# Kernel tuning notes

Hardware: AMD Instinct MI355X
Metric: run time of the kernel (lower is better)

## Reference

```python
import jax, jax.numpy as jnp
import numpy as np

N_LAYERS = 2
K_NEIGHBOURS = 30  # graph_top_K keeps k_neighbours + 1 entries per row
EPS = 1e-12        # torch F.normalize eps


def setup_inputs() -> dict:
    key = jax.random.key(0)
    k1, k2 = jax.random.split(key)
    N, d = 8192, 512
    x = jax.random.normal(k1, (N, d), dtype=jnp.float32)
    W = jax.random.normal(k2, (N_LAYERS, d, d), dtype=jnp.float32) * 0.02
    b = jnp.zeros((N_LAYERS, d), dtype=jnp.float32)
    return {"x": x, "W": W, "b": b}


def reference(x, W, b):
    # MLP: interval_forward -- relu between layers, linear on last layer
    h = x
    for i in range(N_LAYERS - 1):
        h = jax.nn.relu(h @ W[i].T + b[i])
    h = h @ W[N_LAYERS - 1].T + b[N_LAYERS - 1]

    # F.normalize(h, dim=-1, p=2)
    norm = jnp.linalg.norm(h, axis=-1, keepdims=True)
    h = h / jnp.maximum(norm, EPS)

    # cal_similarity_graph: dense N x N cosine similarity
    sim = h @ h.T  # [N, N]

    # graph_top_K(sim, k+1): keep top-(k+1) values per row, zero elsewhere
    k = K_NEIGHBOURS + 1
    vals, idx = jax.lax.top_k(sim, k)  # [N, k]
    N = sim.shape[0]
    masked = jnp.zeros_like(sim).at[jnp.arange(N)[:, None], idx].set(vals)

    # apply_non_linearity(x, 'relu', slope, alpha) -> relu
    return jax.nn.relu(masked)
```

## Files before the change

kernel.cpp:

```cpp
#include <hip/hip_runtime.h>
#include <hip/hip_bf16.h>

typedef __attribute__((ext_vector_type(8))) short bf16x8;
typedef __attribute__((ext_vector_type(8))) unsigned short u16x8;
typedef __attribute__((ext_vector_type(4))) float f32x4;

__global__ __launch_bounds__(256)
void gemm_nt(const float* __restrict__ A, const float* __restrict__ B,
             const float* __restrict__ bias, float* __restrict__ C,
             int M, int N, int K, int do_relu)
{
    constexpr int KS = 16;
    constexpr int LDT = 132;
    __shared__ float As[KS * LDT];
    __shared__ float Bs[KS * LDT];

    const int t    = threadIdx.x;
    const int row0 = blockIdx.y * 128;
    const int col0 = blockIdx.x * 128;
    const int tm   = t & 15;
    const int tn   = t >> 4;
    const int lrow = t >> 2;
    const int lk   = (t & 3) << 2;

    const float* Ap0 = A + (size_t)(row0 + lrow)      * K + lk;
    const float* Ap1 = A + (size_t)(row0 + lrow + 64) * K + lk;
    const float* Bp0 = B + (size_t)(col0 + lrow)      * K + lk;
    const float* Bp1 = B + (size_t)(col0 + lrow + 64) * K + lk;

    float4 a0 = *(const float4*)(Ap0);
    float4 a1 = *(const float4*)(Ap1);
    float4 b0 = *(const float4*)(Bp0);
    float4 b1 = *(const float4*)(Bp1);

    float acc[8][8];
#pragma unroll
    for (int i = 0; i < 8; ++i)
#pragma unroll
        for (int j = 0; j < 8; ++j) acc[i][j] = 0.f;

    for (int k0 = 0; k0 < K; k0 += KS) {
        __syncthreads();
        As[(lk + 0) * LDT + lrow] = a0.x;
        As[(lk + 1) * LDT + lrow] = a0.y;
        As[(lk + 2) * LDT + lrow] = a0.z;
        As[(lk + 3) * LDT + lrow] = a0.w;
        As[(lk + 0) * LDT + lrow + 64] = a1.x;
        As[(lk + 1) * LDT + lrow + 64] = a1.y;
        As[(lk + 2) * LDT + lrow + 64] = a1.z;
        As[(lk + 3) * LDT + lrow + 64] = a1.w;
        Bs[(lk + 0) * LDT + lrow] = b0.x;
        Bs[(lk + 1) * LDT + lrow] = b0.y;
        Bs[(lk + 2) * LDT + lrow] = b0.z;
        Bs[(lk + 3) * LDT + lrow] = b0.w;
        Bs[(lk + 0) * LDT + lrow + 64] = b1.x;
        Bs[(lk + 1) * LDT + lrow + 64] = b1.y;
        Bs[(lk + 2) * LDT + lrow + 64] = b1.z;
        Bs[(lk + 3) * LDT + lrow + 64] = b1.w;
        __syncthreads();
        if (k0 + KS < K) {
            a0 = *(const float4*)(Ap0 + k0 + KS);
            a1 = *(const float4*)(Ap1 + k0 + KS);
            b0 = *(const float4*)(Bp0 + k0 + KS);
            b1 = *(const float4*)(Bp1 + k0 + KS);
        }
#pragma unroll
        for (int kk = 0; kk < KS; ++kk) {
            const float4 av0 = *(const float4*)&As[kk * LDT + 8 * tm];
            const float4 av1 = *(const float4*)&As[kk * LDT + 8 * tm + 4];
            const float4 bv0 = *(const float4*)&Bs[kk * LDT + 8 * tn];
            const float4 bv1 = *(const float4*)&Bs[kk * LDT + 8 * tn + 4];
            const float a[8] = {av0.x, av0.y, av0.z, av0.w, av1.x, av1.y, av1.z, av1.w};
            const float bb[8] = {bv0.x, bv0.y, bv0.z, bv0.w, bv1.x, bv1.y, bv1.z, bv1.w};
#pragma unroll
            for (int i = 0; i < 8; ++i)
#pragma unroll
                for (int j = 0; j < 8; ++j)
                    acc[i][j] += a[i] * bb[j];
        }
    }

#pragma unroll
    for (int i = 0; i < 8; ++i) {
        const int r = row0 + 8 * tm + i;
        float* Crow = C + (size_t)r * N + col0 + 8 * tn;
        float o[8];
#pragma unroll
        for (int j = 0; j < 8; ++j) o[j] = acc[i][j];
        if (bias) {
#pragma unroll
            for (int j = 0; j < 8; ++j) o[j] += bias[col0 + 8 * tn + j];
        }
        if (do_relu) {
#pragma unroll
            for (int j = 0; j < 8; ++j) o[j] = fmaxf(o[j], 0.f);
        }
        float4 o0 = {o[0], o[1], o[2], o[3]};
        float4 o1 = {o[4], o[5], o[6], o[7]};
        *(float4*)(Crow)     = o0;
        *(float4*)(Crow + 4) = o1;
    }
}

__global__ __launch_bounds__(128)
void rownorm_split(const float* __restrict__ in, unsigned short* __restrict__ Hhi,
                   unsigned short* __restrict__ Hmid, unsigned short* __restrict__ Hlo)
{
    __shared__ float s[2];
    const int r = blockIdx.x, t = threadIdx.x;
    const float4 v = ((const float4*)(in + (size_t)r * 512))[t];
    float ss = v.x * v.x + v.y * v.y + v.z * v.z + v.w * v.w;
#pragma unroll
    for (int off = 32; off; off >>= 1) ss += __shfl_down(ss, off);
    if ((t & 63) == 0) s[t >> 6] = ss;
    __syncthreads();
    const float den = fmaxf(sqrtf(s[0] + s[1]), 1e-12f);
    const float f[4] = {v.x / den, v.y / den, v.z / den, v.w / den};
    ushort4 uh, um, ul;
    unsigned short* ph = (unsigned short*)&uh;
    unsigned short* pm = (unsigned short*)&um;
    unsigned short* pl = (unsigned short*)&ul;
#pragma unroll
    for (int j = 0; j < 4; ++j) {
        const __hip_bfloat16 h = __float2bfloat16(f[j]);
        const float fh = __bfloat162float(h);
        const float r1 = f[j] - fh;
        const __hip_bfloat16 m = __float2bfloat16(r1);
        const float fm = __bfloat162float(m);
        const float r2 = r1 - fm;
        const __hip_bfloat16 l = __float2bfloat16(r2);
        ph[j] = *(const unsigned short*)&h;
        pm[j] = *(const unsigned short*)&m;
        pl[j] = *(const unsigned short*)&l;
    }
    const size_t o = (size_t)r * 512 + 4 * t;
    *(ushort4*)(Hhi  + o) = uh;
    *(ushort4*)(Hmid + o) = um;
    *(ushort4*)(Hlo  + o) = ul;
}

__global__ __launch_bounds__(256)
void gemm_sym_mfma(const unsigned short* __restrict__ Hhi,
                   const unsigned short* __restrict__ Hmid,
                   const unsigned short* __restrict__ Hlo,
                   float* __restrict__ C, int Nn)
{
    constexpr int K  = 512;
    constexpr int KC = 32;
    constexpr int LR = 40;
    __shared__ unsigned short lds[6 * 128 * LR];

    const int q = blockIdx.x;
    int ct = (int)((sqrtf(8.0f * (float)q + 1.0f) - 1.0f) * 0.5f);
    while ((ct + 1) * (ct + 2) / 2 <= q) ++ct;
    while (ct * (ct + 1) / 2 > q) --ct;
    const int rt = q - ct * (ct + 1) / 2;
    const int row0 = rt * 128;
    const int col0 = ct * 128;

    const int t    = threadIdx.x;
    const int lane = t & 63;
    const int wid  = t >> 6;
    const int wr   = (wid >> 1) * 64;
    const int wc   = (wid & 1) * 64;

    const int r  = t >> 1;
    const int kh = (t & 1) * 16;
    const unsigned short* srcs[6] = {
        Hhi  + (size_t)(row0 + r) * K, Hmid + (size_t)(row0 + r) * K, Hlo + (size_t)(row0 + r) * K,
        Hhi  + (size_t)(col0 + r) * K, Hmid + (size_t)(col0 + r) * K, Hlo + (size_t)(col0 + r) * K };

    u16x8 pf[12];
#pragma unroll
    for (int a = 0; a < 6; ++a) {
        pf[2 * a]     = *(const u16x8*)(srcs[a] + kh);
        pf[2 * a + 1] = *(const u16x8*)(srcs[a] + kh + 8);
    }

    f32x4 acc[4][4];
#pragma unroll
    for (int i = 0; i < 4; ++i)
#pragma unroll
        for (int j = 0; j < 4; ++j) acc[i][j] = (f32x4){0.f, 0.f, 0.f, 0.f};

    const int fro = (lane & 15) * LR + 8 * (lane >> 4);

    for (int k0 = 0; k0 < K; k0 += KC) {
        __syncthreads();
#pragma unroll
        for (int a = 0; a < 6; ++a) {
            *(u16x8*)&lds[a * 128 * LR + r * LR + kh]     = pf[2 * a];
            *(u16x8*)&lds[a * 128 * LR + r * LR + kh + 8] = pf[2 * a + 1];
        }
        __syncthreads();
        if (k0 + KC < K) {
#pragma unroll
            for (int a = 0; a < 6; ++a) {
                pf[2 * a]     = *(const u16x8*)(srcs[a] + k0 + KC + kh);
                pf[2 * a + 1] = *(const u16x8*)(srcs[a] + k0 + KC + kh + 8);
            }
        }
        bf16x8 af[3][4], bf[3][4];
#pragma unroll
        for (int p = 0; p < 3; ++p)
#pragma unroll
            for (int ti = 0; ti < 4; ++ti) {
                af[p][ti] = *(const bf16x8*)&lds[p * 128 * LR + (wr + ti * 16) * LR + fro];
                bf[p][ti] = *(const bf16x8*)&lds[(3 + p) * 128 * LR + (wc + ti * 16) * LR + fro];
            }
#pragma unroll
        for (int ti = 0; ti < 4; ++ti)
#pragma unroll
            for (int tj = 0; tj < 4; ++tj) {
                f32x4 c = acc[ti][tj];
                c = __builtin_amdgcn_mfma_f32_16x16x32_bf16(af[0][ti], bf[0][tj], c, 0, 0, 0);
                c = __builtin_amdgcn_mfma_f32_16x16x32_bf16(af[0][ti], bf[1][tj], c, 0, 0, 0);
                c = __builtin_amdgcn_mfma_f32_16x16x32_bf16(af[1][ti], bf[0][tj], c, 0, 0, 0);
                c = __builtin_amdgcn_mfma_f32_16x16x32_bf16(af[1][ti], bf[1][tj], c, 0, 0, 0);
                c = __builtin_amdgcn_mfma_f32_16x16x32_bf16(af[0][ti], bf[2][tj], c, 0, 0, 0);
                c = __builtin_amdgcn_mfma_f32_16x16x32_bf16(af[2][ti], bf[0][tj], c, 0, 0, 0);
                acc[ti][tj] = c;
            }
    }

    const int crow = (lane >> 4) * 4;
    const int ccol = lane & 15;
#pragma unroll
    for (int ti = 0; ti < 4; ++ti)
#pragma unroll
        for (int tj = 0; tj < 4; ++tj)
#pragma unroll
            for (int qq = 0; qq < 4; ++qq) {
                const int rr = row0 + wr + ti * 16 + crow + qq;
                const int cc = col0 + wc + tj * 16 + ccol;
                C[(size_t)rr * Nn + cc] = acc[ti][tj][qq];
            }
    if (ct != rt) {
#pragma unroll
        for (int ti = 0; ti < 4; ++ti)
#pragma unroll
            for (int tj = 0; tj < 4; ++tj)
#pragma unroll
                for (int qq = 0; qq < 4; ++qq) {
                    const int rr = row0 + wr + ti * 16 + crow + qq;
                    const int cc = col0 + wc + tj * 16 + ccol;
                    C[(size_t)cc * Nn + rr] = acc[ti][tj][qq];
                }
    }
}

__global__ __launch_bounds__(128)
void rownorm(const float* __restrict__ in, float* __restrict__ out)
{
    __shared__ float s[2];
    const int r = blockIdx.x, t = threadIdx.x;
    const float4 v = ((const float4*)(in + (size_t)r * 512))[t];
    float ss = v.x * v.x + v.y * v.y + v.z * v.z + v.w * v.w;
#pragma unroll
    for (int off = 32; off; off >>= 1) ss += __shfl_down(ss, off);
    if ((t & 63) == 0) s[t >> 6] = ss;
    __syncthreads();
    const float den = fmaxf(sqrtf(s[0] + s[1]), 1e-12f);
    float4 o;
    o.x = v.x / den; o.y = v.y / den; o.z = v.z / den; o.w = v.w / den;
    ((float4*)(out + (size_t)r * 512))[t] = o;
}

__global__ __launch_bounds__(256)
void gemm_syn(const float* __restrict__ H, float* __restrict__ C, int Nn, int K)
{
    constexpr int KS = 16;
    constexpr int LDT = 132;
    __shared__ float As[KS * LDT];
    __shared__ float Bs[KS * LDT];

    const int q = blockIdx.x;
    int ct = (int)((sqrtf(8.0f * (float)q + 1.0f) - 1.0f) * 0.5f);
    while ((ct + 1) * (ct + 2) / 2 <= q) ++ct;
    while (ct * (ct + 1) / 2 > q) --ct;
    const int rt = q - ct * (ct + 1) / 2;
    const int row0 = rt * 128;
    const int col0 = ct * 128;

    const int t    = threadIdx.x;
    const int tm   = t & 15;
    const int tn   = t >> 4;
    const int lrow = t >> 2;
    const int lk   = (t & 3) << 2;

    const float* Ap0 = H + (size_t)(row0 + lrow)      * K + lk;
    const float* Ap1 = H + (size_t)(row0 + lrow + 64) * K + lk;
    const float* Bp0 = H + (size_t)(col0 + lrow)      * K + lk;
    const float* Bp1 = H + (size_t)(col0 + lrow + 64) * K + lk;

    float4 a0 = *(const float4*)(Ap0);
    float4 a1 = *(const float4*)(Ap1);
    float4 b0 = *(const float4*)(Bp0);
    float4 b1 = *(const float4*)(Bp1);

    float acc[8][8];
#pragma unroll
    for (int i = 0; i < 8; ++i)
#pragma unroll
        for (int j = 0; j < 8; ++j) acc[i][j] = 0.f;

    for (int k0 = 0; k0 < K; k0 += KS) {
        __syncthreads();
        As[(lk + 0) * LDT + lrow] = a0.x;
        As[(lk + 1) * LDT + lrow] = a0.y;
        As[(lk + 2) * LDT + lrow] = a0.z;
        As[(lk + 3) * LDT + lrow] = a0.w;
        As[(lk + 0) * LDT + lrow + 64] = a1.x;
        As[(lk + 1) * LDT + lrow + 64] = a1.y;
        As[(lk + 2) * LDT + lrow + 64] = a1.z;
        As[(lk + 3) * LDT + lrow + 64] = a1.w;
        Bs[(lk + 0) * LDT + lrow] = b0.x;
        Bs[(lk + 1) * LDT + lrow] = b0.y;
        Bs[(lk + 2) * LDT + lrow] = b0.z;
        Bs[(lk + 3) * LDT + lrow] = b0.w;
        Bs[(lk + 0) * LDT + lrow + 64] = b1.x;
        Bs[(lk + 1) * LDT + lrow + 64] = b1.y;
        Bs[(lk + 2) * LDT + lrow + 64] = b1.z;
        Bs[(lk + 3) * LDT + lrow + 64] = b1.w;
        __syncthreads();
        if (k0 + KS < K) {
            a0 = *(const float4*)(Ap0 + k0 + KS);
            a1 = *(const float4*)(Ap1 + k0 + KS);
            b0 = *(const float4*)(Bp0 + k0 + KS);
            b1 = *(const float4*)(Bp1 + k0 + KS);
        }
#pragma unroll
        for (int kk = 0; kk < KS; ++kk) {
            const float4 av0 = *(const float4*)&As[kk * LDT + 4 * tm];
            const float4 av1 = *(const float4*)&As[kk * LDT + 4 * tm + 64];
            const float4 bv0 = *(const float4*)&Bs[kk * LDT + 4 * tn];
            const float4 bv1 = *(const float4*)&Bs[kk * LDT + 4 * tn + 64];
            const float a[8] = {av0.x, av0.y, av0.z, av0.w, av1.x, av1.y, av1.z, av1.w};
            const float bb[8] = {bv0.x, bv0.y, bv0.z, bv0.w, bv1.x, bv1.y, bv1.z, bv1.w};
#pragma unroll
            for (int i = 0; i < 8; ++i)
#pragma unroll
                for (int j = 0; j < 8; ++j)
                    acc[i][j] += a[i] * bb[j];
        }
    }

#pragma unroll
    for (int ih = 0; ih < 2; ++ih)
#pragma unroll
    for (int i2 = 0; i2 < 4; ++i2) {
        const int rr = row0 + ih * 64 + 4 * tm + i2;
        float* Crow = C + (size_t)rr * Nn + col0;
        const int ia = ih * 4 + i2;
        float4 o0 = {acc[ia][0], acc[ia][1], acc[ia][2], acc[ia][3]};
        float4 o1 = {acc[ia][4], acc[ia][5], acc[ia][6], acc[ia][7]};
        *(float4*)(Crow + 4 * tn)      = o0;
        *(float4*)(Crow + 64 + 4 * tn) = o1;
    }
    if (ct != rt) {
#pragma unroll
        for (int jh = 0; jh < 2; ++jh)
#pragma unroll
        for (int j2 = 0; j2 < 4; ++j2) {
            const int rr = col0 + jh * 64 + 4 * tn + j2;
            float* Crow = C + (size_t)rr * Nn + row0;
            const int ja = jh * 4 + j2;
            float4 o0 = {acc[0][ja], acc[1][ja], acc[2][ja], acc[3][ja]};
            float4 o1 = {acc[4][ja], acc[5][ja], acc[6][ja], acc[7][ja]};
            *(float4*)(Crow + 4 * tm)      = o0;
            *(float4*)(Crow + 64 + 4 * tm) = o1;
        }
    }
}

__device__ __forceinline__ unsigned mono(float f)
{
    unsigned b = __float_as_uint(f);
    return (b & 0x80000000u) ? ~b : (b | 0x80000000u);
}
__device__ __forceinline__ float unmono(unsigned u)
{
    return __uint_as_float((u & 0x80000000u) ? (u ^ 0x80000000u) : ~u);
}

__global__ __launch_bounds__(256)
void topk_radix(float* __restrict__ sim)
{
    constexpr int NC = 8192;
    __shared__ unsigned keys[NC];
    __shared__ unsigned bins4[4][256];
    __shared__ unsigned sh_pref[2], sh_targ[2];
    __shared__ int tie_idx[256];
    __shared__ int tie_cnt, sh_tie_thr;

    const int t = threadIdx.x;
    const int lane = t & 63;
    const int wid = t >> 6;
    float* row = sim + (size_t)blockIdx.x * NC;

    if (t == 0) { sh_pref[0] = 0u; sh_targ[0] = 31u; tie_cnt = 0; }
#pragma unroll
    for (int j = 0; j < 8; ++j) {
        const int i0 = 4 * (t + 256 * j);
        const float4 v = *(const float4*)&row[i0];
        uint4 k;
        k.x = mono(v.x); k.y = mono(v.y); k.z = mono(v.z); k.w = mono(v.w);
        *(uint4*)&keys[i0] = k;
    }
    __syncthreads();

    unsigned prefmask = 0u;
    for (int p = 0; p < 4; ++p) {
        const int shift = 24 - 8 * p;
#pragma unroll
        for (int w = 0; w < 4; ++w) bins4[w][t] = 0u;
        __syncthreads();
        const unsigned prefix = sh_pref[p & 1];
        const unsigned target = sh_targ[p & 1];
        for (int j = 0; j < 32; ++j) {
            const unsigned u = keys[t + 256 * j];
            if ((u & prefmask) == prefix)
                atomicAdd(&bins4[wid][(u >> shift) & 255u], 1u);
        }
        __syncthreads();
        if (wid == 0) {
            unsigned bb[4];
#pragma unroll
            for (int jj = 0; jj < 4; ++jj)
                bb[jj] = bins4[0][4 * lane + jj] + bins4[1][4 * lane + jj]
                       + bins4[2][4 * lane + jj] + bins4[3][4 * lane + jj];
            const unsigned tot = bb[0] + bb[1] + bb[2] + bb[3];
            unsigned s = tot;
#pragma unroll
            for (int off = 1; off < 64; off <<= 1) {
                const unsigned o = __shfl_down(s, off);
                if (lane + off < 64) s += o;
            }
            unsigned cge[5];
            cge[4] = s - tot;
            cge[3] = cge[4] + bb[3];
            cge[2] = cge[3] + bb[2];
            cge[1] = cge[2] + bb[1];
            cge[0] = cge[1] + bb[0];
#pragma unroll
            for (int jj = 0; jj < 4; ++jj) {
                if (cge[jj] >= target && cge[jj + 1] < target) {
                    sh_pref[(p + 1) & 1] = prefix | ((unsigned)(4 * lane + jj) << shift);
                    sh_targ[(p + 1) & 1] = target - cge[jj + 1];
                }
            }
        }
        prefmask |= (255u << shift);
        __syncthreads();
    }
    const unsigned uc = sh_pref[0];
    const int m = (int)sh_targ[0];

    for (int j = 0; j < 32; ++j) {
        const int i = t + 256 * j;
        if (keys[i] == uc) {
            const int p = atomicAdd(&tie_cnt, 1);
            if (p < 256) tie_idx[p] = i;
        }
    }
    __syncthreads();
    if (t == 0) {
        int n = tie_cnt < 256 ? tie_cnt : 256;
        for (int a = 1; a < n; ++a) {
            const int key = tie_idx[a];
            int c = a - 1;
            while (c >= 0 && tie_idx[c] > key) { tie_idx[c + 1] = tie_idx[c]; --c; }
            tie_idx[c + 1] = key;
        }
        const int mm = (m <= n ? m : n);
        sh_tie_thr = tie_idx[mm - 1];
    }
    __syncthreads();
    const int tie_thr = sh_tie_thr;

#pragma unroll
    for (int j = 0; j < 8; ++j) {
        const int i0 = 4 * (t + 256 * j);
        const uint4 k = *(const uint4*)&keys[i0];
        float4 v;
        v.x = (k.x > uc || (k.x == uc && i0 + 0 <= tie_thr)) ? fmaxf(unmono(k.x), 0.f) : 0.f;
        v.y = (k.y > uc || (k.y == uc && i0 + 1 <= tie_thr)) ? fmaxf(unmono(k.y), 0.f) : 0.f;
        v.z = (k.z > uc || (k.z == uc && i0 + 2 <= tie_thr)) ? fmaxf(unmono(k.z), 0.f) : 0.f;
        v.w = (k.w > uc || (k.w == uc && i0 + 3 <= tie_thr)) ? fmaxf(unmono(k.w), 0.f) : 0.f;
        *(float4*)&row[i0] = v;
    }
}

extern "C" void kernel_launch(void* const* d_in, const int* in_sizes, int n_in,
                              void* d_out, int out_size, void* d_ws, size_t ws_size,
                              hipStream_t stream)
{
    const float* x = (const float*)d_in[0];
    const float* W = (const float*)d_in[1];
    const float* b = (const float*)d_in[2];
    float* out = (float*)d_out;

    const int N = 8192, D = 512;
    const int T = N / 128;

    float* h1 = out;
    float* h2 = out + (size_t)N * D;

    dim3 tb(256);
    gemm_nt<<<dim3(D / 128, N / 128), tb, 0, stream>>>(x,  W,                 b,     h1, N, D, D, 1);
    gemm_nt<<<dim3(D / 128, N / 128), tb, 0, stream>>>(h1, W + (size_t)D * D, b + D, h2, N, D, D, 0);

    const size_t split_bytes = (size_t)3 * N * D * sizeof(unsigned short);
    if (ws_size >= split_bytes) {
        unsigned short* Hhi  = (unsigned short*)d_ws;
        unsigned short* Hmid = Hhi  + (size_t)N * D;
        unsigned short* Hlo  = Hmid + (size_t)N * D;
        rownorm_split<<<N, 128, 0, stream>>>(h2, Hhi, Hmid, Hlo);
        gemm_sym_mfma<<<T * (T + 1) / 2, tb, 0, stream>>>(Hhi, Hmid, Hlo, out, N);
    } else {
        float* hn = (float*)d_ws;
        rownorm<<<N, 128, 0, stream>>>(h2, hn);
        gemm_syn<<<T * (T + 1) / 2, tb, 0, stream>>>(hn, out, N, D);
    }
    topk_radix<<<N, tb, 0, stream>>>(out);
}
```

Before: 929.6 us.

## Replace shared-memory radix top-k with register-resident bitwise threshold search

The per-row top-k kernel no longer stages 8192 keys in shared memory or builds 8-bit histograms with shared atomics. Each thread keeps its 32 keys in registers and finds the 31st-largest key by a 32-step bit-by-bit search, using wave shuffles plus a small cross-wave sum at each step. This removes the 32KB shared buffer and the atomic contention, which should raise occupancy. In exchange it runs 32 barrier rounds instead of 4 histogram passes, and each round does 32 compares per thread.

Result: faster. 758.3 us (-18.4%).

```diff
diff --git a/kernel.cpp b/kernel.cpp
--- a/kernel.cpp
+++ b/kernel.cpp
@@ -373,9 +373,8 @@
     }
 }
 
-__device__ __forceinline__ unsigned mono(float f)
-{
-    unsigned b = __float_as_uint(f);
+__device__ __forceinline__ unsigned monou(unsigned b)
+{
     return (b & 0x80000000u) ? ~b : (b | 0x80000000u);
 }
 __device__ __forceinline__ float unmono(unsigned u)
@@ -384,85 +383,70 @@
 }
 
 __global__ __launch_bounds__(256)
-void topk_radix(float* __restrict__ sim)
+void topk_bits(float* __restrict__ sim)
 {
     constexpr int NC = 8192;
-    __shared__ unsigned keys[NC];
-    __shared__ unsigned bins4[4][256];
-    __shared__ unsigned sh_pref[2], sh_targ[2];
+    constexpr unsigned KSEL = 31;
+    __shared__ unsigned wsum[2][4];
     __shared__ int tie_idx[256];
-    __shared__ int tie_cnt, sh_tie_thr;
+    __shared__ int tie_cnt, sh_thr;
 
     const int t = threadIdx.x;
     const int lane = t & 63;
     const int wid = t >> 6;
     float* row = sim + (size_t)blockIdx.x * NC;
 
-    if (t == 0) { sh_pref[0] = 0u; sh_targ[0] = 31u; tie_cnt = 0; }
+    if (t == 0) tie_cnt = 0;
+
+    unsigned k[8][4];
 #pragma unroll
     for (int j = 0; j < 8; ++j) {
-        const int i0 = 4 * (t + 256 * j);
-        const float4 v = *(const float4*)&row[i0];
-        uint4 k;
-        k.x = mono(v.x); k.y = mono(v.y); k.z = mono(v.z); k.w = mono(v.w);
-        *(uint4*)&keys[i0] = k;
-    }
-    __syncthreads();
-
-    unsigned prefmask = 0u;
-    for (int p = 0; p < 4; ++p) {
-        const int shift = 24 - 8 * p;
-#pragma unroll
-        for (int w = 0; w < 4; ++w) bins4[w][t] = 0u;
-        __syncthreads();
-        const unsigned prefix = sh_pref[p & 1];
-        const unsigned target = sh_targ[p & 1];
-        for (int j = 0; j < 32; ++j) {
-            const unsigned u = keys[t + 256 * j];
-            if ((u & prefmask) == prefix)
-                atomicAdd(&bins4[wid][(u >> shift) & 255u], 1u);
-        }
-        __syncthreads();
-        if (wid == 0) {
-            unsigned bb[4];
-#pragma unroll
-            for (int jj = 0; jj < 4; ++jj)
-                bb[jj] = bins4[0][4 * lane + jj] + bins4[1][4 * lane + jj]
-                       + bins4[2][4 * lane + jj] + bins4[3][4 * lane + jj];
-            const unsigned tot = bb[0] + bb[1] + bb[2] + bb[3];
-            unsigned s = tot;
-#pragma unroll
-            for (int off = 1; off < 64; off <<= 1) {
-                const unsigned o = __shfl_down(s, off);
-                if (lane + off < 64) s += o;
+        const uint4 v = *(const uint4*)&row[4 * (t + 256 * j)];
+        k[j][0] = monou(v.x); k[j][1] = monou(v.y);
+        k[j][2] = monou(v.z); k[j][3] = monou(v.w);
+    }
+
+    unsigned X = 0u;
+    for (int b = 31; b >= 0; --b) {
+        const unsigned cand = X | (1u << b);
+        unsigned c = 0;
+#pragma unroll
+        for (int j = 0; j < 8; ++j)
+#pragma unroll
+            for (int e = 0; e < 4; ++e)
+                c += (k[j][e] >= cand) ? 1u : 0u;
+#pragma unroll
+        for (int off = 32; off; off >>= 1) c += __shfl_xor(c, off);
+        if (lane == 0) wsum[b & 1][wid] = c;
+        __syncthreads();
+        const unsigned tot = wsum[b & 1][0] + wsum[b & 1][1]
+                           + wsum[b & 1][2] + wsum[b & 1][3];
+        if (tot >= KSEL) X = cand;
+    }
+    const unsigned uc = X;
+
+    {
+        unsigned c = 0;
+#pragma unroll
+        for (int j = 0; j < 8; ++j)
+#pragma unroll
+            for (int e = 0; e < 4; ++e)
+                c += (k[j][e] > uc) ? 1u : 0u;
+#pragma unroll
+        for (int off = 32; off; off >>= 1) c += __shfl_xor(c, off);
+        if (lane == 0) wsum[1][wid] = c;
+        __syncthreads();
+    }
+    const int m = (int)(KSEL - (wsum[1][0] + wsum[1][1] + wsum[1][2] + wsum[1][3]));
+
+#pragma unroll
+    for (int j = 0; j < 8; ++j)
+#pragma unroll
+        for (int e = 0; e < 4; ++e)
+            if (k[j][e] == uc) {
+                const int p = atomicAdd(&tie_cnt, 1);
+                if (p < 256) tie_idx[p] = 4 * (t + 256 * j) + e;
             }
-            unsigned cge[5];
-            cge[4] = s - tot;
-            cge[3] = cge[4] + bb[3];
-            cge[2] = cge[3] + bb[2];
-            cge[1] = cge[2] + bb[1];
-            cge[0] = cge[1] + bb[0];
-#pragma unroll
-            for (int jj = 0; jj < 4; ++jj) {
-                if (cge[jj] >= target && cge[jj + 1] < target) {
-                    sh_pref[(p + 1) & 1] = prefix | ((unsigned)(4 * lane + jj) << shift);
-                    sh_targ[(p + 1) & 1] = target - cge[jj + 1];
-                }
-            }
-        }
-        prefmask |= (255u << shift);
-        __syncthreads();
-    }
-    const unsigned uc = sh_pref[0];
-    const int m = (int)sh_targ[0];
-
-    for (int j = 0; j < 32; ++j) {
-        const int i = t + 256 * j;
-        if (keys[i] == uc) {
-            const int p = atomicAdd(&tie_cnt, 1);
-            if (p < 256) tie_idx[p] = i;
-        }
-    }
     __syncthreads();
     if (t == 0) {
         int n = tie_cnt < 256 ? tie_cnt : 256;
@@ -473,20 +457,19 @@
             tie_idx[c + 1] = key;
         }
         const int mm = (m <= n ? m : n);
-        sh_tie_thr = tie_idx[mm - 1];
+        sh_thr = tie_idx[mm - 1];
     }
     __syncthreads();
-    const int tie_thr = sh_tie_thr;
+    const int tie_thr = sh_thr;
 
 #pragma unroll
     for (int j = 0; j < 8; ++j) {
         const int i0 = 4 * (t + 256 * j);
-        const uint4 k = *(const uint4*)&keys[i0];
         float4 v;
-        v.x = (k.x > uc || (k.x == uc && i0 + 0 <= tie_thr)) ? fmaxf(unmono(k.x), 0.f) : 0.f;
-        v.y = (k.y > uc || (k.y == uc && i0 + 1 <= tie_thr)) ? fmaxf(unmono(k.y), 0.f) : 0.f;
-        v.z = (k.z > uc || (k.z == uc && i0 + 2 <= tie_thr)) ? fmaxf(unmono(k.z), 0.f) : 0.f;
-        v.w = (k.w > uc || (k.w == uc && i0 + 3 <= tie_thr)) ? fmaxf(unmono(k.w), 0.f) : 0.f;
+        v.x = (k[j][0] > uc || (k[j][0] == uc && i0 + 0 <= tie_thr)) ? fmaxf(unmono(k[j][0]), 0.f) : 0.f;
+        v.y = (k[j][1] > uc || (k[j][1] == uc && i0 + 1 <= tie_thr)) ? fmaxf(unmono(k[j][1]), 0.f) : 0.f;
+        v.z = (k[j][2] > uc || (k[j][2] == uc && i0 + 2 <= tie_thr)) ? fmaxf(unmono(k[j][2]), 0.f) : 0.f;
+        v.w = (k[j][3] > uc || (k[j][3] == uc && i0 + 3 <= tie_thr)) ? fmaxf(unmono(k[j][3]), 0.f) : 0.f;
         *(float4*)&row[i0] = v;
     }
 }
@@ -522,5 +505,5 @@
         rownorm<<<N, 128, 0, stream>>>(h2, hn);
         gemm_syn<<<T * (T + 1) / 2, tb, 0, stream>>>(hn, out, N, D);
     }
-    topk_radix<<<N, tb, 0, stream>>>(out);
-}
+    topk_bits<<<N, tb, 0, stream>>>(out);
+}
```
